# Kernel tuning notes

Hardware: AMD Instinct MI355X
Metric: run time of the kernel (lower is better)

## Reference

```python
import jax, jax.numpy as jnp
import numpy as np

B, S_DIM, A_DIM = 8192, 39, 4
D_IN = S_DIM + A_DIM  # 43
F = 1024              # n_features width
E = 8                 # n_experts
C = 10                # n_contexts
N_OUT = 1


def setup_inputs() -> dict:
    key = jax.random.key(0)
    ks = jax.random.split(key, 12)
    inp = {
        "state": jax.random.normal(ks[0], (B, S_DIM), jnp.float32),
        "action": jax.random.normal(ks[1], (B, A_DIM), jnp.float32),
        "c": jax.random.randint(ks[2], (B,), 0, C, jnp.int32),
        # per-expert backbone params (InputLayer+ParallelLayer => E independent MLPs)
        "W0": jax.random.normal(ks[3], (E, D_IN, F), jnp.float32) * 0.05,
        "b0": jnp.zeros((E, F), jnp.float32),
        "W1": jax.random.normal(ks[4], (E, F, F), jnp.float32) * 0.03,
        "b1": jnp.zeros((E, F), jnp.float32),
        # task encoder: Linear(n_contexts -> n_experts, bias=False), weight [E, C]
        "Wte": jax.random.normal(ks[5], (E, C), jnp.float32) * 0.3,
        # per-context output heads: Linear(F -> 1)
        "Wh": jax.random.normal(ks[6], (C, F, N_OUT), jnp.float32) * 0.03,
        "bh": jnp.zeros((C, N_OUT), jnp.float32),
    }
    return inp


def reference(state, action, c, W0, b0, W1, b1, Wte, Wh, bh):
    # mixture weights: one_hot(c) @ Wte^T  ==  Wte[:, c]^T  -> [B, E]
    w = Wte.T[c]                                            # [B, E]
    sa = jnp.concatenate([state, action], axis=1)           # [B, D_IN]
    # per-expert backbone MLP (ReLU after each layer, incl. last since activation='ReLU')
    h = jax.nn.relu(jnp.einsum('bi,eio->ebo', sa, W0) + b0[:, None, :])   # [E, B, F]
    h = jax.nn.relu(jnp.einsum('ebi,eio->ebo', h, W1) + b1[:, None, :])   # [E, B, F]
    feats = jnp.transpose(h, (1, 0, 2))                     # [B, E, F]
    feats = jax.nn.relu(feats)                              # agg_activation[0]
    mixed = jnp.einsum('be,bef->bf', w, feats)              # [B, F]
    mixed = jax.nn.relu(mixed)                              # agg_activation[1]
    # context-routed heads: gather each sample's head params (same math as the
    # unique-context scatter loop in the original)
    q = jnp.einsum('bf,bfo->bo', mixed, Wh[c]) + bh[c]      # [B, 1]
    return jnp.squeeze(q, axis=-1)                          # [B]
```

## Files before the change

kernel.cpp:

```cpp
#include <hip/hip_runtime.h>
#include <hip/hip_bf16.h>
#include <stdint.h>

typedef __attribute__((ext_vector_type(8))) __bf16 bf16x8;
typedef __attribute__((ext_vector_type(4))) float f32x4;

__device__ __forceinline__ unsigned short f2b(float f) {
    return __builtin_bit_cast(unsigned short, __float2bfloat16(f));
}
__device__ __forceinline__ float b2f(unsigned int u) {
    return __builtin_bit_cast(float, u << 16);
}

__device__ __forceinline__ void gload_lds16(const void* g, void* l) {
    __builtin_amdgcn_global_load_lds(
        (__attribute__((address_space(1))) void*)(uintptr_t)g,
        (__attribute__((address_space(3))) void*)l,
        16, 0, 0);
}

#define MFMA16(a, b, c) __builtin_amdgcn_mfma_f32_16x16x32_bf16((a), (b), (c), 0, 0, 0)


__global__ void k_prep_sa(const float* __restrict__ state, const float* __restrict__ action,
                          const int* __restrict__ c, const float* __restrict__ Wte,
                          unsigned short* __restrict__ SA, float* __restrict__ wmix, int B) {
    int b = blockIdx.x * 256 + threadIdx.x;
    if (b >= B) return;
    unsigned short* row = SA + (size_t)b * 64;
#pragma unroll
    for (int i = 0; i < 39; ++i) row[i] = f2b(state[(size_t)b * 39 + i]);
#pragma unroll
    for (int i = 0; i < 4; ++i) row[39 + i] = f2b(action[(size_t)b * 4 + i]);
#pragma unroll
    for (int i = 43; i < 64; ++i) row[i] = 0;
    int ctx = c[b];
#pragma unroll
    for (int e = 0; e < 8; ++e) wmix[(size_t)b * 8 + e] = Wte[e * 10 + ctx];
}

__global__ void k_prep_w0t(const float* __restrict__ W0, unsigned short* __restrict__ W0T) {
    int idx = blockIdx.x * 256 + threadIdx.x;
    int e = idx >> 10, f = idx & 1023;
    unsigned short* dst = W0T + (size_t)idx * 64;
#pragma unroll 1
    for (int k = 0; k < 43; ++k) dst[k] = f2b(W0[((size_t)e * 43 + k) * 1024 + f]);
#pragma unroll
    for (int k = 43; k < 64; ++k) dst[k] = 0;
}

__global__ void k_prep_w1t(const float* __restrict__ W1, unsigned short* __restrict__ W1T) {
    __shared__ float t[64][65];
    int k0 = blockIdx.x * 64, n0 = blockIdx.y * 64, e = blockIdx.z;
    int tid = threadIdx.x;
    int cl = tid & 63, rg = tid >> 6;
    const float* src = W1 + ((size_t)e * 1024 + k0) * 1024 + n0;
#pragma unroll
    for (int i = 0; i < 16; ++i) {
        int kr = rg * 16 + i;
        t[kr][cl] = src[(size_t)kr * 1024 + cl];
    }
    __syncthreads();
    int nl = tid >> 2, kg = tid & 3;
    unsigned short* dst = W1T + ((size_t)e * 1024 + n0 + nl) * 1024 + k0 + kg * 16;
#pragma unroll
    for (int j = 0; j < 16; ++j) dst[j] = f2b(t[kg * 16 + j][nl]);
}

__global__ __launch_bounds__(256, 2)
void k_layer0(const unsigned short* __restrict__ SA,
              const unsigned short* __restrict__ W0T,
              const float* __restrict__ b0,
              unsigned short* __restrict__ H0,
              int Btot) {
    __shared__ unsigned short As[128 * 64];
    __shared__ unsigned short Bs[128 * 64];
    int bm = blockIdx.x, bn = blockIdx.y, e = blockIdx.z;
    int tid = threadIdx.x, lane = tid & 63;
    int wv = tid >> 6, wr = wv >> 1, wc = wv & 1;
    int l15 = lane & 15, kg = lane >> 4;

    const char* Ag = (const char*)(SA + (size_t)(bm * 128) * 64);
    const char* Bg = (const char*)(W0T + ((size_t)e * 1024 + bn * 128) * 64);
#pragma unroll
    for (int it = 0; it < 4; ++it) {
        int off = tid * 16 + it * 4096;
        gload_lds16(Ag + off, (char*)As + off);
        gload_lds16(Bg + off, (char*)Bs + off);
    }
    __syncthreads();

    f32x4 acc[4][4];
#pragma unroll
    for (int mi = 0; mi < 4; ++mi)
#pragma unroll
        for (int ni = 0; ni < 4; ++ni) acc[mi][ni] = (f32x4)0.0f;

#pragma unroll
    for (int ks = 0; ks < 2; ++ks) {
        bf16x8 af[4], bv[4];
#pragma unroll
        for (int mi = 0; mi < 4; ++mi)
            af[mi] = *(const bf16x8*)&As[(wr * 64 + mi * 16 + l15) * 64 + ks * 32 + kg * 8];
#pragma unroll
        for (int ni = 0; ni < 4; ++ni)
            bv[ni] = *(const bf16x8*)&Bs[(wc * 64 + ni * 16 + l15) * 64 + ks * 32 + kg * 8];
#pragma unroll
        for (int mi = 0; mi < 4; ++mi)
#pragma unroll
            for (int ni = 0; ni < 4; ++ni)
                acc[mi][ni] = MFMA16(af[mi], bv[ni], acc[mi][ni]);
    }

    float b0v[4];
#pragma unroll
    for (int ni = 0; ni < 4; ++ni)
        b0v[ni] = b0[e * 1024 + bn * 128 + wc * 64 + ni * 16 + l15];
#pragma unroll
    for (int mi = 0; mi < 4; ++mi)
#pragma unroll
        for (int ni = 0; ni < 4; ++ni)
#pragma unroll
            for (int j = 0; j < 4; ++j) {
                int rloc = bm * 128 + wr * 64 + mi * 16 + kg * 4 + j;
                int col = bn * 128 + wc * 64 + ni * 16 + l15;
                float h = fmaxf(acc[mi][ni][j] + b0v[ni], 0.0f);
                H0[((size_t)e * Btot + rloc) * 1024 + col] = f2b(h);
            }
}

__global__ __launch_bounds__(512, 2)
void k_gemm_h1(const unsigned short* __restrict__ H0,
               const unsigned short* __restrict__ W1T,
               const float* __restrict__ b1,
               uint2* __restrict__ H1F,
               int Btot, int row0, int nbm) {
    __shared__ unsigned short SH[65536];

    int wg = blockIdx.x;
    int c8 = wg & 7, r = wg >> 3;
    int bn = r & 3, pg = r >> 2;
    int pair = c8 + 8 * pg;
    int e = pair / nbm, bm = pair - e * nbm;

    int tid = threadIdx.x, lane = tid & 63;
    int wv = tid >> 6;
    int wr = wv >> 2, wc = wv & 3;
    int l15 = lane & 15, kg = lane >> 4;
    int k0s = (kg * 16) ^ ((l15 & 7) << 4);
    int k1s = (64 + kg * 16) ^ ((l15 & 7) << 4);

    int flat = tid * 16;
    int srow = flat >> 7;
    int scol = (flat & 127) ^ ((srow & 7) << 4);

    const char* h0e = (const char*)H0 + ((size_t)e * Btot + row0 + (size_t)bm * 256) * 2048;
    const char* w1e = (const char*)W1T + ((size_t)e * 1024 + (size_t)bn * 256) * 2048;
    char* Asb = (char*)SH;
    char* Bsb = (char*)SH + 65536;

    int aRow[8], bRow[4];
#pragma unroll
    for (int m = 0; m < 8; ++m) aRow[m] = (((m >> 2) * 64) + (m & 3) * 16 + l15) * 128;
#pragma unroll
    for (int n = 0; n < 4; ++n) bRow[n] = ((wc & 1) * 64 + n * 16 + l15) * 128;

    float b1v[4];
#pragma unroll
    for (int n = 0; n < 4; ++n)
        b1v[n] = b1[e * 1024 + bn * 256 + wc * 64 + n * 16 + l15];
    asm volatile("s_waitcnt vmcnt(0)" ::: "memory");

    auto STAGE_B2 = [&](int tt) {
        int k0b = tt << 7;
        char* dstb = Bsb + (tt & 1) * 32768;
        const char* s0 = w1e + k0b;
        gload_lds16(s0 + (size_t)srow * 2048 + scol, dstb + flat);
        gload_lds16(s0 + (size_t)(srow + 64) * 2048 + scol, dstb + flat + 8192);
        const char* s1 = w1e + (size_t)128 * 2048 + k0b;
        gload_lds16(s1 + (size_t)srow * 2048 + scol, dstb + 16384 + flat);
        gload_lds16(s1 + (size_t)(srow + 64) * 2048 + scol, dstb + 16384 + flat + 8192);
    };
    auto STAGE_A2 = [&](int tt) {
        int k0b = tt << 7;
        char* dsta = Asb + (tt & 1) * 32768;
        const char* s0 = h0e + k0b;
        gload_lds16(s0 + (size_t)srow * 2048 + scol, dsta + flat);
        gload_lds16(s0 + (size_t)(srow + 64) * 2048 + scol, dsta + flat + 8192);
        const char* s1 = h0e + (size_t)128 * 2048 + k0b;
        gload_lds16(s1 + (size_t)srow * 2048 + scol, dsta + 16384 + flat);
        gload_lds16(s1 + (size_t)(srow + 64) * 2048 + scol, dsta + 16384 + flat + 8192);
    };

    const int NT = 16;

    STAGE_B2(0); STAGE_A2(0);
    STAGE_B2(1); STAGE_A2(1);
    asm volatile("s_waitcnt vmcnt(8)" ::: "memory");
    __builtin_amdgcn_s_barrier();

    f32x4 acc[8][4];
#pragma unroll
    for (int m = 0; m < 8; ++m)
#pragma unroll
        for (int n = 0; n < 4; ++n) acc[m][n] = (f32x4)0.0f;

    bf16x8 af0[4][2], af1[4][2], bf0[2][2], bf1[2][2];

    {
        const char* Ab = Asb + (0 * 2 + wr) * 16384;
        const char* Bb = Bsb + (0 * 2 + (wc >> 1)) * 16384;
#pragma unroll
        for (int mi = 0; mi < 4; ++mi) {
            af0[mi][0] = *(const bf16x8*)(Ab + aRow[mi] + k0s);
            af0[mi][1] = *(const bf16x8*)(Ab + aRow[mi] + k1s);
        }
#pragma unroll
        for (int ni = 0; ni < 2; ++ni) {
            bf0[ni][0] = *(const bf16x8*)(Bb + bRow[ni] + k0s);
            bf0[ni][1] = *(const bf16x8*)(Bb + bRow[ni] + k1s);
        }
    }

#pragma unroll 1
    for (int t = 0; t < NT; ++t) {
        int buf = t & 1, nb = buf ^ 1;
        const char* Ab = Asb + (buf * 2 + wr) * 16384;
        const char* Bb = Bsb + (buf * 2 + (wc >> 1)) * 16384;
        const char* AbN = Asb + (nb * 2 + wr) * 16384;
        const char* BbN = Bsb + (nb * 2 + (wc >> 1)) * 16384;

#pragma unroll
        for (int ni = 0; ni < 2; ++ni) {
            bf1[ni][0] = *(const bf16x8*)(Bb + bRow[2 + ni] + k0s);
            bf1[ni][1] = *(const bf16x8*)(Bb + bRow[2 + ni] + k1s);
        }
        asm volatile("s_waitcnt lgkmcnt(4)" ::: "memory");
        __builtin_amdgcn_sched_barrier(0);
        __builtin_amdgcn_s_setprio(1);
#pragma unroll
        for (int k = 0; k < 2; ++k)
#pragma unroll
            for (int mi = 0; mi < 4; ++mi)
#pragma unroll
                for (int ni = 0; ni < 2; ++ni)
                    acc[mi][ni] = MFMA16(af0[mi][k], bf0[ni][k], acc[mi][ni]);
        __builtin_amdgcn_s_setprio(0);
        __builtin_amdgcn_sched_barrier(0);
        __builtin_amdgcn_s_barrier();

#pragma unroll
        for (int mi = 0; mi < 4; ++mi) {
            af1[mi][0] = *(const bf16x8*)(Ab + aRow[4 + mi] + k0s);
            af1[mi][1] = *(const bf16x8*)(Ab + aRow[4 + mi] + k1s);
        }
        asm volatile("s_waitcnt lgkmcnt(8)" ::: "memory");
        __builtin_amdgcn_sched_barrier(0);
        __builtin_amdgcn_s_setprio(1);
#pragma unroll
        for (int k = 0; k < 2; ++k)
#pragma unroll
            for (int mi = 0; mi < 4; ++mi)
#pragma unroll
                for (int ni = 0; ni < 2; ++ni)
                    acc[mi][2 + ni] = MFMA16(af0[mi][k], bf1[ni][k], acc[mi][2 + ni]);
        __builtin_amdgcn_s_setprio(0);
        __builtin_amdgcn_sched_barrier(0);
        __builtin_amdgcn_s_barrier();

        if (t + 2 < NT) STAGE_B2(t + 2);
        asm volatile("s_waitcnt lgkmcnt(0)" ::: "memory");
        __builtin_amdgcn_sched_barrier(0);
        __builtin_amdgcn_s_setprio(1);
#pragma unroll
        for (int k = 0; k < 2; ++k)
#pragma unroll
            for (int mi = 0; mi < 4; ++mi)
#pragma unroll
                for (int ni = 0; ni < 2; ++ni)
                    acc[4 + mi][ni] = MFMA16(af1[mi][k], bf0[ni][k], acc[4 + mi][ni]);
        __builtin_amdgcn_s_setprio(0);
        __builtin_amdgcn_sched_barrier(0);
        if (t + 2 < NT)
            asm volatile("s_waitcnt vmcnt(4)" ::: "memory");
        else
            asm volatile("s_waitcnt vmcnt(0)" ::: "memory");
        __builtin_amdgcn_s_barrier();

        if (t + 1 < NT) {
#pragma unroll
            for (int mi = 0; mi < 4; ++mi) {
                af0[mi][0] = *(const bf16x8*)(AbN + aRow[mi] + k0s);
                af0[mi][1] = *(const bf16x8*)(AbN + aRow[mi] + k1s);
            }
#pragma unroll
            for (int ni = 0; ni < 2; ++ni) {
                bf0[ni][0] = *(const bf16x8*)(BbN + bRow[ni] + k0s);
                bf0[ni][1] = *(const bf16x8*)(BbN + bRow[ni] + k1s);
            }
        }
        if (t + 2 < NT) STAGE_A2(t + 2);
        __builtin_amdgcn_sched_barrier(0);
        __builtin_amdgcn_s_setprio(1);
#pragma unroll
        for (int k = 0; k < 2; ++k)
#pragma unroll
            for (int mi = 0; mi < 4; ++mi)
#pragma unroll
                for (int ni = 0; ni < 2; ++ni)
                    acc[4 + mi][2 + ni] = MFMA16(af1[mi][k], bf1[ni][k], acc[4 + mi][2 + ni]);
        __builtin_amdgcn_s_setprio(0);
        __builtin_amdgcn_sched_barrier(0);
        __builtin_amdgcn_s_barrier();
    }

    uint2* h1b = H1F + (size_t)((e * nbm + bm) * 4 + bn) * 16384;
#pragma unroll
    for (int m = 0; m < 8; ++m)
#pragma unroll
        for (int n = 0; n < 4; ++n) {
            float v0 = fmaxf(acc[m][n][0] + b1v[n], 0.0f);
            float v1 = fmaxf(acc[m][n][1] + b1v[n], 0.0f);
            float v2 = fmaxf(acc[m][n][2] + b1v[n], 0.0f);
            float v3 = fmaxf(acc[m][n][3] + b1v[n], 0.0f);
            uint2 u;
            u.x = (unsigned int)f2b(v0) | ((unsigned int)f2b(v1) << 16);
            u.y = (unsigned int)f2b(v2) | ((unsigned int)f2b(v3) << 16);
            h1b[((wv * 8 + m) * 4 + n) * 64 + lane] = u;
        }
}

__global__ __launch_bounds__(256)
void k_mixhead(const uint2* __restrict__ H1F, const float* __restrict__ wmix,
               const float* __restrict__ Wh, const float* __restrict__ bh,
               const int* __restrict__ c, float* __restrict__ q,
               int Bc, int row0, int nbm) {
    int lane = threadIdx.x & 63;
    int rg = blockIdx.x * 4 + (threadIdx.x >> 6);
    int rbase = rg * 4;
    if (rbase >= Bc) return;
    int bm = rbase >> 8;
    int lrow = rbase & 255;
    int wr = lrow >> 7, m = (lrow >> 4) & 7, kg = (lrow >> 2) & 3;
    int wc = lane >> 4, l15 = lane & 15;

    float w[4][8];
#pragma unroll
    for (int j = 0; j < 4; ++j)
#pragma unroll
        for (int e = 0; e < 8; ++e)
            w[j][e] = wmix[(size_t)(row0 + rbase + j) * 8 + e];

    float acc[4][16];
#pragma unroll
    for (int j = 0; j < 4; ++j)
#pragma unroll
        for (int s = 0; s < 16; ++s) acc[j][s] = 0.0f;

    int ubase = (((wr * 4 + wc) * 8 + m) * 4) * 64 + kg * 16 + l15;

#pragma unroll 1
    for (int e = 0; e < 8; ++e) {
        size_t eb = (size_t)(e * nbm + bm) * 4;
#pragma unroll
        for (int bn = 0; bn < 4; ++bn) {
            const uint2* blk = H1F + (eb + bn) * 16384;
#pragma unroll
            for (int n = 0; n < 4; ++n) {
                uint2 u = blk[ubase + n * 64];
                float v0 = b2f(u.x & 0xffffu), v1 = b2f(u.x >> 16);
                float v2 = b2f(u.y & 0xffffu), v3 = b2f(u.y >> 16);
                int s = bn * 4 + n;
                acc[0][s] += w[0][e] * v0;
                acc[1][s] += w[1][e] * v1;
                acc[2][s] += w[2][e] * v2;
                acc[3][s] += w[3][e] * v3;
            }
        }
    }

#pragma unroll
    for (int j = 0; j < 4; ++j) {
        int grow = row0 + rbase + j;
        int ctx = c[grow];
        const float* whp = Wh + (size_t)ctx * 1024;
        float s = 0.0f;
#pragma unroll
        for (int slot = 0; slot < 16; ++slot) {
            int f = (slot >> 2) * 256 + wc * 64 + (slot & 3) * 16 + l15;
            s += fmaxf(acc[j][slot], 0.0f) * whp[f];
        }
#pragma unroll
        for (int off = 32; off > 0; off >>= 1) s += __shfl_down(s, off);
        if (lane == 0) q[grow] = s + bh[ctx];
    }
}

extern "C" void kernel_launch(void* const* d_in, const int* in_sizes, int n_in,
                              void* d_out, int out_size, void* d_ws, size_t ws_size,
                              hipStream_t stream) {
    const float* state  = (const float*)d_in[0];
    const float* action = (const float*)d_in[1];
    const int*   c      = (const int*)d_in[2];
    const float* W0     = (const float*)d_in[3];
    const float* b0     = (const float*)d_in[4];
    const float* W1     = (const float*)d_in[5];
    const float* b1     = (const float*)d_in[6];
    const float* Wte    = (const float*)d_in[7];
    const float* Wh     = (const float*)d_in[8];
    const float* bh     = (const float*)d_in[9];
    float* q = (float*)d_out;
    int B = in_sizes[2];

    char* p = (char*)d_ws;
    unsigned short* W1T = (unsigned short*)p; p += (size_t)8 * 1024 * 1024 * 2;
    unsigned short* W0T = (unsigned short*)p; p += (size_t)8 * 1024 * 64 * 2;
    unsigned short* SA  = (unsigned short*)p; p += (size_t)B * 64 * 2;
    float* wmix         = (float*)p;          p += (size_t)B * 8 * 4;
    size_t fixed = (size_t)(p - (char*)d_ws);

    size_t h0sz = (size_t)8 * B * 1024 * 2;
    unsigned short* H0 = (unsigned short*)p; p += h0sz;

    int Bc = B;
    while (Bc > 256 && fixed + h0sz + (size_t)8 * Bc * 1024 * 2 > ws_size) Bc >>= 1;
    uint2* H1F = (uint2*)p;

    k_prep_sa<<<(B + 255) / 256, 256, 0, stream>>>(state, action, c, Wte, SA, wmix, B);
    k_prep_w0t<<<(8 * 1024) / 256, 256, 0, stream>>>(W0, W0T);
    k_prep_w1t<<<dim3(16, 16, 8), 256, 0, stream>>>(W1, W1T);
    k_layer0<<<dim3(B / 128, 8, 8), 256, 0, stream>>>(SA, W0T, b0, H0, B);

    for (int row0 = 0; row0 < B; row0 += Bc) {
        int nbm = Bc / 256;
        k_gemm_h1<<<nbm * 32, 512, 0, stream>>>(H0, W1T, b1, H1F, B, row0, nbm);
        k_mixhead<<<Bc / 16, 256, 0, stream>>>(H1F, wmix, Wh, bh, c, q, Bc, row0, nbm);
    }
}
```

Baseline: 236.5 us.

## Fuse expert mixing into layer-1 GEMM, loop over experts inside tile

The layer-1 GEMM now iterates over all 8 experts inside each workgroup, applying bias, ReLU and the per-row mixture weight to accumulate a mixed result in registers. This removes the bf16 H1 intermediate for all experts (8×B×1024) and its write and re-read by the mix kernel. Only the fp32 mixed tensor is written, and a simple per-row head kernel reduces it with the context head. Tiles change to 256x128 with 256 threads and one block per CU, doubling accumulator registers (acc plus mix). This risks lower occupancy and a grid of 256 workgroups, which may underfill the GPU.

```diff
diff --git a/kernel.cpp b/kernel.cpp
--- a/kernel.cpp
+++ b/kernel.cpp
@@ -7,9 +7,6 @@
 
 __device__ __forceinline__ unsigned short f2b(float f) {
     return __builtin_bit_cast(unsigned short, __float2bfloat16(f));
-}
-__device__ __forceinline__ float b2f(unsigned int u) {
-    return __builtin_bit_cast(float, u << 16);
 }
 
 __device__ __forceinline__ void gload_lds16(const void* g, void* l) {
@@ -129,23 +126,26 @@
             }
 }
 
-__global__ __launch_bounds__(512, 2)
-void k_gemm_h1(const unsigned short* __restrict__ H0,
-               const unsigned short* __restrict__ W1T,
-               const float* __restrict__ b1,
-               uint2* __restrict__ H1F,
-               int Btot, int row0, int nbm) {
-    __shared__ unsigned short SH[65536];
+__global__ __launch_bounds__(256, 1)
+void k_fused(const unsigned short* __restrict__ H0,
+             const unsigned short* __restrict__ W1T,
+             const float* __restrict__ b1,
+             const float* __restrict__ wmix,
+             float* __restrict__ mixed,
+             int Btot) {
+    __shared__ unsigned short As[2][256 * 64];
+    __shared__ unsigned short Bs[2][128 * 64];
+    __shared__ float wmixLds[256 * 8];
+    __shared__ float b1Lds[8 * 128];
 
     int wg = blockIdx.x;
-    int c8 = wg & 7, r = wg >> 3;
-    int bn = r & 3, pg = r >> 2;
-    int pair = c8 + 8 * pg;
-    int e = pair / nbm, bm = pair - e * nbm;
+    int x8 = wg & 7, j = wg >> 3;
+    int bm = x8 + ((j >> 3) << 3);
+    int bn = j & 7;
 
     int tid = threadIdx.x, lane = tid & 63;
     int wv = tid >> 6;
-    int wr = wv >> 2, wc = wv & 3;
+    int wr = wv >> 1, wc = wv & 1;
     int l15 = lane & 15, kg = lane >> 4;
     int k0s = (kg * 16) ^ ((l15 & 7) << 4);
     int k1s = (64 + kg * 16) ^ ((l15 & 7) << 4);
@@ -154,62 +154,61 @@
     int srow = flat >> 7;
     int scol = (flat & 127) ^ ((srow & 7) << 4);
 
-    const char* h0e = (const char*)H0 + ((size_t)e * Btot + row0 + (size_t)bm * 256) * 2048;
-    const char* w1e = (const char*)W1T + ((size_t)e * 1024 + (size_t)bn * 256) * 2048;
-    char* Asb = (char*)SH;
-    char* Bsb = (char*)SH + 65536;
+    const char* h0b = (const char*)H0 + (size_t)(bm * 256) * 2048;
+    const char* w1b = (const char*)W1T + (size_t)(bn * 128) * 2048;
+    size_t eA = (size_t)Btot * 2048;
+    char* Asb = (char*)As;
+    char* Bsb = (char*)Bs;
 
     int aRow[8], bRow[4];
 #pragma unroll
-    for (int m = 0; m < 8; ++m) aRow[m] = (((m >> 2) * 64) + (m & 3) * 16 + l15) * 128;
-#pragma unroll
-    for (int n = 0; n < 4; ++n) bRow[n] = ((wc & 1) * 64 + n * 16 + l15) * 128;
-
-    float b1v[4];
-#pragma unroll
-    for (int n = 0; n < 4; ++n)
-        b1v[n] = b1[e * 1024 + bn * 256 + wc * 64 + n * 16 + l15];
-    asm volatile("s_waitcnt vmcnt(0)" ::: "memory");
-
-    auto STAGE_B2 = [&](int tt) {
-        int k0b = tt << 7;
-        char* dstb = Bsb + (tt & 1) * 32768;
-        const char* s0 = w1e + k0b;
-        gload_lds16(s0 + (size_t)srow * 2048 + scol, dstb + flat);
-        gload_lds16(s0 + (size_t)(srow + 64) * 2048 + scol, dstb + flat + 8192);
-        const char* s1 = w1e + (size_t)128 * 2048 + k0b;
-        gload_lds16(s1 + (size_t)srow * 2048 + scol, dstb + 16384 + flat);
-        gload_lds16(s1 + (size_t)(srow + 64) * 2048 + scol, dstb + 16384 + flat + 8192);
+    for (int m = 0; m < 8; ++m) aRow[m] = (wr * 128 + m * 16 + l15) * 128;
+#pragma unroll
+    for (int n = 0; n < 4; ++n) bRow[n] = (wc * 64 + n * 16 + l15) * 128;
+
+    for (int idx = tid; idx < 2048; idx += 256) {
+        int r = idx >> 3, e = idx & 7;
+        wmixLds[idx] = wmix[(size_t)(bm * 256 + r) * 8 + e];
+    }
+    for (int idx = tid; idx < 1024; idx += 256)
+        b1Lds[idx] = b1[(idx >> 7) * 1024 + bn * 128 + (idx & 127)];
+    __syncthreads();
+
+    auto STAGE_A = [&](int tt) {
+        int e = tt >> 4, k0b = (tt & 15) << 7;
+        const char* s = h0b + (size_t)e * eA + k0b;
+        char* d = Asb + (tt & 1) * 32768;
+#pragma unroll
+        for (int i = 0; i < 8; ++i)
+            gload_lds16(s + (size_t)(srow + i * 32) * 2048 + scol, d + flat + i * 4096);
     };
-    auto STAGE_A2 = [&](int tt) {
-        int k0b = tt << 7;
-        char* dsta = Asb + (tt & 1) * 32768;
-        const char* s0 = h0e + k0b;
-        gload_lds16(s0 + (size_t)srow * 2048 + scol, dsta + flat);
-        gload_lds16(s0 + (size_t)(srow + 64) * 2048 + scol, dsta + flat + 8192);
-        const char* s1 = h0e + (size_t)128 * 2048 + k0b;
-        gload_lds16(s1 + (size_t)srow * 2048 + scol, dsta + 16384 + flat);
-        gload_lds16(s1 + (size_t)(srow + 64) * 2048 + scol, dsta + 16384 + flat + 8192);
+    auto STAGE_B = [&](int tt) {
+        int e = tt >> 4, k0b = (tt & 15) << 7;
+        const char* s = w1b + (size_t)e * (1024 * 2048) + k0b;
+        char* d = Bsb + (tt & 1) * 16384;
+#pragma unroll
+        for (int i = 0; i < 4; ++i)
+            gload_lds16(s + (size_t)(srow + i * 32) * 2048 + scol, d + flat + i * 4096);
     };
 
-    const int NT = 16;
-
-    STAGE_B2(0); STAGE_A2(0);
-    STAGE_B2(1); STAGE_A2(1);
-    asm volatile("s_waitcnt vmcnt(8)" ::: "memory");
+    const int NT = 128;
+
+    STAGE_B(0); STAGE_A(0);
+    STAGE_B(1); STAGE_A(1);
+    asm volatile("s_waitcnt vmcnt(12)" ::: "memory");
     __builtin_amdgcn_s_barrier();
 
-    f32x4 acc[8][4];
+    f32x4 acc[8][4], mix[8][4];
 #pragma unroll
     for (int m = 0; m < 8; ++m)
 #pragma unroll
-        for (int n = 0; n < 4; ++n) acc[m][n] = (f32x4)0.0f;
+        for (int n = 0; n < 4; ++n) { acc[m][n] = (f32x4)0.0f; mix[m][n] = (f32x4)0.0f; }
 
     bf16x8 af0[4][2], af1[4][2], bf0[2][2], bf1[2][2];
 
     {
-        const char* Ab = Asb + (0 * 2 + wr) * 16384;
-        const char* Bb = Bsb + (0 * 2 + (wc >> 1)) * 16384;
+        const char* Ab = Asb;
+        const char* Bb = Bsb;
 #pragma unroll
         for (int mi = 0; mi < 4; ++mi) {
             af0[mi][0] = *(const bf16x8*)(Ab + aRow[mi] + k0s);
@@ -225,10 +224,10 @@
 #pragma unroll 1
     for (int t = 0; t < NT; ++t) {
         int buf = t & 1, nb = buf ^ 1;
-        const char* Ab = Asb + (buf * 2 + wr) * 16384;
-        const char* Bb = Bsb + (buf * 2 + (wc >> 1)) * 16384;
-        const char* AbN = Asb + (nb * 2 + wr) * 16384;
-        const char* BbN = Bsb + (nb * 2 + (wc >> 1)) * 16384;
+        const char* Ab = Asb + buf * 32768;
+        const char* Bb = Bsb + buf * 16384;
+        const char* AbN = Asb + nb * 32768;
+        const char* BbN = Bsb + nb * 16384;
 
 #pragma unroll
         for (int ni = 0; ni < 2; ++ni) {
@@ -268,7 +267,7 @@
         __builtin_amdgcn_sched_barrier(0);
         __builtin_amdgcn_s_barrier();
 
-        if (t + 2 < NT) STAGE_B2(t + 2);
+        if (t + 2 < NT) STAGE_B(t + 2);
         asm volatile("s_waitcnt lgkmcnt(0)" ::: "memory");
         __builtin_amdgcn_sched_barrier(0);
         __builtin_amdgcn_s_setprio(1);
@@ -299,7 +298,7 @@
                 bf0[ni][1] = *(const bf16x8*)(BbN + bRow[ni] + k1s);
             }
         }
-        if (t + 2 < NT) STAGE_A2(t + 2);
+        if (t + 2 < NT) STAGE_A(t + 2);
         __builtin_amdgcn_sched_barrier(0);
         __builtin_amdgcn_s_setprio(1);
 #pragma unroll
@@ -312,88 +311,60 @@
         __builtin_amdgcn_s_setprio(0);
         __builtin_amdgcn_sched_barrier(0);
         __builtin_amdgcn_s_barrier();
-    }
-
-    uint2* h1b = H1F + (size_t)((e * nbm + bm) * 4 + bn) * 16384;
+
+        if ((t & 15) == 15) {
+            int e = t >> 4;
+            float b1v[4];
+#pragma unroll
+            for (int n = 0; n < 4; ++n)
+                b1v[n] = b1Lds[e * 128 + wc * 64 + n * 16 + l15];
+#pragma unroll
+            for (int m = 0; m < 8; ++m)
+#pragma unroll
+                for (int j = 0; j < 4; ++j) {
+                    int lrow = wr * 128 + m * 16 + kg * 4 + j;
+                    float w = wmixLds[lrow * 8 + e];
+#pragma unroll
+                    for (int n = 0; n < 4; ++n) {
+                        float h = fmaxf(acc[m][n][j] + b1v[n], 0.0f);
+                        mix[m][n][j] += w * h;
+                        acc[m][n][j] = 0.0f;
+                    }
+                }
+        }
+    }
+
 #pragma unroll
     for (int m = 0; m < 8; ++m)
 #pragma unroll
-        for (int n = 0; n < 4; ++n) {
-            float v0 = fmaxf(acc[m][n][0] + b1v[n], 0.0f);
-            float v1 = fmaxf(acc[m][n][1] + b1v[n], 0.0f);
-            float v2 = fmaxf(acc[m][n][2] + b1v[n], 0.0f);
-            float v3 = fmaxf(acc[m][n][3] + b1v[n], 0.0f);
-            uint2 u;
-            u.x = (unsigned int)f2b(v0) | ((unsigned int)f2b(v1) << 16);
-            u.y = (unsigned int)f2b(v2) | ((unsigned int)f2b(v3) << 16);
-            h1b[((wv * 8 + m) * 4 + n) * 64 + lane] = u;
-        }
-}
-
-__global__ __launch_bounds__(256)
-void k_mixhead(const uint2* __restrict__ H1F, const float* __restrict__ wmix,
-               const float* __restrict__ Wh, const float* __restrict__ bh,
-               const int* __restrict__ c, float* __restrict__ q,
-               int Bc, int row0, int nbm) {
+        for (int n = 0; n < 4; ++n)
+#pragma unroll
+            for (int j = 0; j < 4; ++j) {
+                int row = bm * 256 + wr * 128 + m * 16 + kg * 4 + j;
+                int col = bn * 128 + wc * 64 + n * 16 + l15;
+                mixed[(size_t)row * 1024 + col] = fmaxf(mix[m][n][j], 0.0f);
+            }
+}
+
+__global__ void k_head(const float* __restrict__ mixed, const float* __restrict__ Wh,
+                       const float* __restrict__ bh, const int* __restrict__ c,
+                       float* __restrict__ q, int Btot) {
+    int row = blockIdx.x * 4 + (threadIdx.x >> 6);
     int lane = threadIdx.x & 63;
-    int rg = blockIdx.x * 4 + (threadIdx.x >> 6);
-    int rbase = rg * 4;
-    if (rbase >= Bc) return;
-    int bm = rbase >> 8;
-    int lrow = rbase & 255;
-    int wr = lrow >> 7, m = (lrow >> 4) & 7, kg = (lrow >> 2) & 3;
-    int wc = lane >> 4, l15 = lane & 15;
-
-    float w[4][8];
-#pragma unroll
-    for (int j = 0; j < 4; ++j)
-#pragma unroll
-        for (int e = 0; e < 8; ++e)
-            w[j][e] = wmix[(size_t)(row0 + rbase + j) * 8 + e];
-
-    float acc[4][16];
-#pragma unroll
-    for (int j = 0; j < 4; ++j)
-#pragma unroll
-        for (int s = 0; s < 16; ++s) acc[j][s] = 0.0f;
-
-    int ubase = (((wr * 4 + wc) * 8 + m) * 4) * 64 + kg * 16 + l15;
-
-#pragma unroll 1
-    for (int e = 0; e < 8; ++e) {
-        size_t eb = (size_t)(e * nbm + bm) * 4;
-#pragma unroll
-        for (int bn = 0; bn < 4; ++bn) {
-            const uint2* blk = H1F + (eb + bn) * 16384;
-#pragma unroll
-            for (int n = 0; n < 4; ++n) {
-                uint2 u = blk[ubase + n * 64];
-                float v0 = b2f(u.x & 0xffffu), v1 = b2f(u.x >> 16);
-                float v2 = b2f(u.y & 0xffffu), v3 = b2f(u.y >> 16);
-                int s = bn * 4 + n;
-                acc[0][s] += w[0][e] * v0;
-                acc[1][s] += w[1][e] * v1;
-                acc[2][s] += w[2][e] * v2;
-                acc[3][s] += w[3][e] * v3;
-            }
-        }
-    }
-
-#pragma unroll
-    for (int j = 0; j < 4; ++j) {
-        int grow = row0 + rbase + j;
-        int ctx = c[grow];
-        const float* whp = Wh + (size_t)ctx * 1024;
-        float s = 0.0f;
-#pragma unroll
-        for (int slot = 0; slot < 16; ++slot) {
-            int f = (slot >> 2) * 256 + wc * 64 + (slot & 3) * 16 + l15;
-            s += fmaxf(acc[j][slot], 0.0f) * whp[f];
-        }
-#pragma unroll
-        for (int off = 32; off > 0; off >>= 1) s += __shfl_down(s, off);
-        if (lane == 0) q[grow] = s + bh[ctx];
-    }
+    if (row >= Btot) return;
+    int ctx = c[row];
+    const float4* m4 = (const float4*)(mixed + (size_t)row * 1024);
+    const float4* w4 = (const float4*)(Wh + (size_t)ctx * 1024);
+    float s = 0.0f;
+#pragma unroll
+    for (int i = 0; i < 4; ++i) {
+        float4 a = m4[lane + i * 64];
+        float4 b = w4[lane + i * 64];
+        s += a.x * b.x + a.y * b.y + a.z * b.z + a.w * b.w;
+    }
+#pragma unroll
+    for (int off = 32; off > 0; off >>= 1) s += __shfl_down(s, off);
+    if (lane == 0) q[row] = s + bh[ctx];
 }
 
 extern "C" void kernel_launch(void* const* d_in, const int* in_sizes, int n_in,
@@ -417,23 +388,13 @@
     unsigned short* W0T = (unsigned short*)p; p += (size_t)8 * 1024 * 64 * 2;
     unsigned short* SA  = (unsigned short*)p; p += (size_t)B * 64 * 2;
     float* wmix         = (float*)p;          p += (size_t)B * 8 * 4;
-    size_t fixed = (size_t)(p - (char*)d_ws);
-
-    size_t h0sz = (size_t)8 * B * 1024 * 2;
-    unsigned short* H0 = (unsigned short*)p; p += h0sz;
-
-    int Bc = B;
-    while (Bc > 256 && fixed + h0sz + (size_t)8 * Bc * 1024 * 2 > ws_size) Bc >>= 1;
-    uint2* H1F = (uint2*)p;
+    unsigned short* H0  = (unsigned short*)p; p += (size_t)8 * B * 1024 * 2;
+    float* mixed        = (float*)p;
 
     k_prep_sa<<<(B + 255) / 256, 256, 0, stream>>>(state, action, c, Wte, SA, wmix, B);
     k_prep_w0t<<<(8 * 1024) / 256, 256, 0, stream>>>(W0, W0T);
     k_prep_w1t<<<dim3(16, 16, 8), 256, 0, stream>>>(W1, W1T);
     k_layer0<<<dim3(B / 128, 8, 8), 256, 0, stream>>>(SA, W0T, b0, H0, B);
-
-    for (int row0 = 0; row0 < B; row0 += Bc) {
-        int nbm = Bc / 256;
-        k_gemm_h1<<<nbm * 32, 512, 0, stream>>>(H0, W1T, b1, H1F, B, row0, nbm);
-        k_mixhead<<<Bc / 16, 256, 0, stream>>>(H1F, wmix, Wh, bh, c, q, Bc, row0, nbm);
-    }
-}
+    k_fused<<<(B / 256) * 8, 256, 0, stream>>>(H0, W1T, b1, wmix, mixed, B);
+    k_head<<<(B + 3) / 4, 256, 0, stream>>>(mixed, Wh, bh, c, q, B);
+}
```

Measured after the change: 424.3 us. 79.4% more time.
